# Performance work log

Measured on AMD Instinct MI355X. Metric: run time of the kernel, lower is better.

The kernel has to match this reference:

```python
import jax, jax.numpy as jnp
import numpy as np

V = 100000   # nodes (atoms)
E = 400000   # directed edges (bonds x2)
N = 74       # node_feat_size
NE = 12      # edge_feat_size
G = 200      # graph_feat_size
L = 2        # num_layers - 1 GNN layers
OUT = 1      # output_size
NG = 4000    # molecules in the batch


def _lin_init(k, fan_in, fan_out):
    s = 1.0 / np.sqrt(fan_in)
    return jax.random.uniform(k, (fan_in, fan_out), jnp.float32, -s, s)


def setup_inputs() -> dict:
    key = jax.random.key(0)
    ks = list(jax.random.split(key, 40))
    p = {}
    # node feats uniform in (0.05, 0.95) so mask = 1/(sum(h[:,-4:])*(1-h[:,0])) - 1 is finite
    p["node_feats"] = jax.random.uniform(ks[0], (V, N), jnp.float32, 0.05, 0.95)
    p["edge_feats"] = jax.random.normal(ks[1], (E, NE), jnp.float32)
    # GetContext params
    p["pn_W"] = _lin_init(ks[2], N, G);            p["pn_b"] = jnp.zeros((G,), jnp.float32)
    p["pe1_W"] = _lin_init(ks[3], N + NE, G);      p["pe1_b"] = jnp.zeros((G,), jnp.float32)
    p["pe2_W"] = _lin_init(ks[4], 2 * G, 1);       p["pe2_b"] = jnp.zeros((1,), jnp.float32)
    p["et_W"] = _lin_init(ks[5], G, G);            p["et_b"] = jnp.zeros((G,), jnp.float32)
    p["gru0_Wih"] = _lin_init(ks[6], G, 3 * G);    p["gru0_Whh"] = _lin_init(ks[7], G, 3 * G)
    p["gru0_bih"] = jnp.zeros((3 * G,), jnp.float32)
    p["gru0_bhh"] = jnp.zeros((3 * G,), jnp.float32)
    # stacked GNNLayer params
    p["gnn_pe_W"] = jnp.stack([_lin_init(ks[8 + l], 2 * G, 1) for l in range(L)])
    p["gnn_pe_b"] = jnp.zeros((L, 1), jnp.float32)
    p["gnn_pn_W"] = jnp.stack([_lin_init(ks[10 + l], G, G) for l in range(L)])
    p["gnn_pn_b"] = jnp.zeros((L, G), jnp.float32)
    p["gnn_gru_Wih"] = jnp.stack([_lin_init(ks[12 + l], G, 3 * G) for l in range(L)])
    p["gnn_gru_Whh"] = jnp.stack([_lin_init(ks[14 + l], G, 3 * G) for l in range(L)])
    p["gnn_gru_bih"] = jnp.zeros((L, 3 * G), jnp.float32)
    p["gnn_gru_bhh"] = jnp.zeros((L, 3 * G), jnp.float32)
    p["pred_W"] = _lin_init(ks[16], G, OUT);       p["pred_b"] = jnp.zeros((OUT,), jnp.float32)
    # graph structure
    p["src"] = jax.random.randint(ks[17], (E,), 0, V)
    p["dst"] = jax.random.randint(ks[18], (E,), 0, V)
    p["graph_ids"] = jnp.arange(V, dtype=jnp.int32) // (V // NG)  # sorted, balanced, non-empty
    p["n_graphs"] = NG
    return p


def _edge_softmax(logits, dst, num_nodes):
    # softmax over incoming edges of each destination node (DGL edge_softmax)
    m = jax.ops.segment_max(logits, dst, num_segments=num_nodes)
    e = jnp.exp(logits - m[dst])
    s = jax.ops.segment_sum(e, dst, num_segments=num_nodes)
    return e / s[dst]


def _gru_cell(x, h, Wih, Whh, bih, bhh):
    gi = x @ Wih + bih
    gh = h @ Whh + bhh
    ir, iz, inn = jnp.split(gi, 3, axis=-1)
    hr, hz, hn = jnp.split(gh, 3, axis=-1)
    r = jax.nn.sigmoid(ir + hr)
    z = jax.nn.sigmoid(iz + hz)
    n = jnp.tanh(inn + r * hn)
    return (1.0 - z) * n + z * h


def _forward(node_feats, edge_feats, pn_W, pn_b, pe1_W, pe1_b, pe2_W, pe2_b,
             et_W, et_b, gru0_Wih, gru0_Whh, gru0_bih, gru0_bhh,
             gnn_pe_W, gnn_pe_b, gnn_pn_W, gnn_pn_b,
             gnn_gru_Wih, gnn_gru_Whh, gnn_gru_bih, gnn_gru_bhh,
             pred_W, pred_b, src, dst, graph_ids, n_graphs):
    Vn = node_feats.shape[0]
    lrelu = jax.nn.leaky_relu  # slope 0.01, matches torch default
    # mask from original node features g.ndata['h']
    mask = jnp.sum(node_feats[:, -4:], axis=1) * (1.0 - node_feats[:, 0])
    mask = 1.0 / mask - 1.0
    # --- GetContext ---
    hv_new = lrelu(node_feats @ pn_W + pn_b)                               # (V, G)
    he1 = lrelu(jnp.concatenate([node_feats[src], edge_feats], 1) @ pe1_W + pe1_b)  # (E, G)
    he2 = jnp.concatenate([hv_new[dst], he1], 1)                           # (E, 2G)
    logits = lrelu(he2 @ pe2_W + pe2_b)                                    # (E, 1)
    a = _edge_softmax(logits, dst, Vn)
    e = a * (he1 @ et_W + et_b)                                            # (E, G)
    c = jax.ops.segment_sum(e, dst, num_segments=Vn)                       # (V, G)
    nf = jax.nn.relu(_gru_cell(jax.nn.elu(c), hv_new,
                               gru0_Wih, gru0_Whh, gru0_bih, gru0_bhh))
    # --- GNN layers ---
    for l in range(gnn_pe_W.shape[0]):
        he = jnp.concatenate([nf[dst], nf[src]], 1)                        # (E, 2G)
        lg = lrelu(he @ gnn_pe_W[l] + gnn_pe_b[l])                         # (E, 1)
        a = _edge_softmax(lg, dst, Vn)
        hvp = nf @ gnn_pn_W[l] + gnn_pn_b[l]                               # (V, G)
        c = jax.ops.segment_sum(hvp[src] * a, dst, num_segments=Vn)        # (V, G)
        nf = jax.nn.relu(_gru_cell(jax.nn.elu(c), nf,
                                   gnn_gru_Wih[l], gnn_gru_Whh[l],
                                   gnn_gru_bih[l], gnn_gru_bhh[l]))
    # --- readout ---
    atom_pka = nf @ pred_W + pred_b                                        # (V, 1)
    atom_pka = -(atom_pka + mask[:, None])
    h_pow = jnp.power(10.0, atom_pka)
    g_feats = -jnp.log10(jax.ops.segment_sum(h_pow, graph_ids, num_segments=n_graphs))
    atom_pka_out = -atom_pka
    return g_feats, atom_pka_out


def reference(node_feats, edge_feats, pn_W, pn_b, pe1_W, pe1_b, pe2_W, pe2_b,
              et_W, et_b, gru0_Wih, gru0_Whh, gru0_bih, gru0_bhh,
              gnn_pe_W, gnn_pe_b, gnn_pn_W, gnn_pn_b,
              gnn_gru_Wih, gnn_gru_Whh, gnn_gru_bih, gnn_gru_bhh,
              pred_W, pred_b, src, dst, graph_ids, n_graphs):
    return _forward(node_feats, edge_feats, pn_W, pn_b, pe1_W, pe1_b, pe2_W, pe2_b,
                    et_W, et_b, gru0_Wih, gru0_Whh, gru0_bih, gru0_bhh,
                    gnn_pe_W, gnn_pe_b, gnn_pn_W, gnn_pn_b,
                    gnn_gru_Wih, gnn_gru_Whh, gnn_gru_bih, gnn_gru_bhh,
                    pred_W, pred_b, src, dst, graph_ids, n_graphs)
```

## Files before the change

kernel.cpp:

```cpp
#include <hip/hip_runtime.h>
#include <hip/hip_bf16.h>
#include <math.h>

#define V_N    100000
#define E_N    400000
#define NFEAT  74
#define NEFEAT 12
#define G_DIM  200
#define LDA    224
#define L_N    2
#define NG_N   4000
#define NROWB  391
#define NROWP  392
#define NSWZ   (NROWP / 8 * 56)
#define NSWZG  (NROWP / 8 * 112)

static inline int cdiv(int a, int b) { return (a + b - 1) / b; }

__device__ __forceinline__ float lrelu_f(float x) { return x > 0.f ? x : 0.01f * x; }
__device__ __forceinline__ float sigmoid_f(float x) { return 1.f / (1.f + expf(-x)); }
__device__ __forceinline__ float elu_f(float x) { return x > 0.f ? x : expm1f(x); }
__device__ __forceinline__ float bf2f(__hip_bfloat16 x) { return __bfloat162float(x); }
__device__ __forceinline__ float bfbits2f(short s) {
    return __uint_as_float(((unsigned)(unsigned short)s) << 16);
}

__device__ __forceinline__ short f2bf(float f) {
    __hip_bfloat16 b = __float2bfloat16(f);
    short s;
    __builtin_memcpy(&s, &b, 2);
    return s;
}

typedef short short8 __attribute__((ext_vector_type(8)));
typedef short short4v __attribute__((ext_vector_type(4)));
typedef float f32x4 __attribute__((ext_vector_type(4)));

#define MFMA16(a, b, c) __builtin_amdgcn_mfma_f32_16x16x32_bf16((a), (b), (c), 0, 0, 0)

#define GLOAD_LDS16(gp, lp) \
    __builtin_amdgcn_global_load_lds((const __attribute__((address_space(1))) void*)(gp), \
                                     (__attribute__((address_space(3))) void*)(lp), 16, 0, 0)

__device__ __forceinline__ void swz_decode7(int lin, int& rowBlk, int& cb)
{
    int grp = lin / 56;
    int rem = lin % 56;
    cb = rem >> 3;
    rowBlk = grp * 8 + (rem & 7);
}

__device__ __forceinline__ void swz_decode14(int lin, int& rowBlk, int& cb)
{
    int grp = lin / 112;
    int rem = lin % 112;
    cb = rem >> 3;
    rowBlk = grp * 8 + (rem & 7);
}

__device__ __forceinline__ f32x4 qcalc(const f32x4* wef, f32x4 ef0, f32x4 ef1, f32x4 ef2)
{
    f32x4 q = ef0[0] * wef[0];
    q += ef0[1] * wef[1];
    q += ef0[2] * wef[2];
    q += ef0[3] * wef[3];
    q += ef1[0] * wef[4];
    q += ef1[1] * wef[5];
    q += ef1[2] * wef[6];
    q += ef1[3] * wef[7];
    q += ef2[0] * wef[8];
    q += ef2[1] * wef[9];
    q += ef2[2] * wef[10];
    q += ef2[3] * wef[11];
    return q;
}

__global__ __launch_bounds__(256)
void fill_kernel(float* __restrict__ p, float v, int n)
{
    int i = blockIdx.x * blockDim.x + threadIdx.x;
    if (i < n) p[i] = v;
}

__global__ __launch_bounds__(256)
void fill_int_kernel(int* __restrict__ p, int v, int n)
{
    int i = blockIdx.x * blockDim.x + threadIdx.x;
    if (i < n) p[i] = v;
}

__global__ __launch_bounds__(256)
void pad_zero_kernel(short* __restrict__ base, size_t VP)
{
    int idx = blockIdx.x * blockDim.x + threadIdx.x;
    if (idx >= 4 * V_N) return;
    int mat = idx / V_N, row = idx % V_N;
    short* p = base + (size_t)mat * VP + (long)row * LDA + G_DIM;
    short8 z = {};
    *(short8*)(p) = z;
    *(short8*)(p + 8) = z;
    *(short8*)(p + 16) = z;
}

__global__ __launch_bounds__(256)
void wprep_kernel(const float* __restrict__ W, short* __restrict__ Wp, int K, int Kpad)
{
    int idx = blockIdx.x * 256 + threadIdx.x;
    if (idx >= 256 * Kpad) return;
    int j = idx / Kpad, k = idx % Kpad;
    float v = (j < G_DIM && k < K) ? W[(long)k * G_DIM + j] : 0.f;
    Wp[idx] = f2bf(v);
}

__global__ __launch_bounds__(256)
void wprep_tiled_kernel(const float* __restrict__ W, short* __restrict__ Wp)
{
    int idx = blockIdx.x * 256 + threadIdx.x;
    if (idx >= 7 * 7 * 1024) return;
    int cb = idx / (7 * 1024);
    int r = idx % (7 * 1024);
    int st = r / 1024;
    int r2 = r % 1024;
    int cc = r2 / 32, kk = r2 % 32;
    int col = cb * 32 + cc, k = st * 32 + kk;
    float v = (col < G_DIM && k < G_DIM) ? W[(long)k * G_DIM + col] : 0.f;
    Wp[idx] = f2bf(v);
}

__global__ __launch_bounds__(256)
void gru_wprep_kernel(const float* __restrict__ Wih, const float* __restrict__ Whh,
                      short* __restrict__ Wp)
{
    int idx = blockIdx.x * 256 + threadIdx.x;
    if (idx >= 14 * 14 * 1536) return;
    int cb = idx / (14 * 1536);
    int r = idx % (14 * 1536);
    int st = r / 1536;
    int r2 = r % 1536;
    int g = r2 / 512;
    int r3 = r2 % 512;
    int cc = r3 / 32, kk = r3 % 32;
    int col = cb * 16 + cc;
    float v = 0.f;
    if (col < G_DIM) {
        if (st < 7) {
            int k = st * 32 + kk;
            if (k < G_DIM) v = Wih[(long)k * (3 * G_DIM) + g * G_DIM + col];
        } else {
            int k = (st - 7) * 32 + kk;
            if (k < G_DIM) v = Whh[(long)k * (3 * G_DIM) + g * G_DIM + col];
        }
    }
    Wp[idx] = f2bf(v);
}

__global__ __launch_bounds__(256)
void hist_kernel(const int* __restrict__ dst, int* __restrict__ deg)
{
    int e = blockIdx.x * blockDim.x + threadIdx.x;
    if (e >= E_N) return;
    atomicAdd(&deg[dst[e]], 1);
}

__global__ __launch_bounds__(256)
void scan1_kernel(const int* __restrict__ deg, int* __restrict__ rp, int* __restrict__ bsum)
{
    __shared__ int s[256];
    int tid = threadIdx.x;
    int v = blockIdx.x * 256 + tid;
    int x = (v < V_N) ? deg[v] : 0;
    s[tid] = x;
    __syncthreads();
    for (int off = 1; off < 256; off <<= 1) {
        int t = (tid >= off) ? s[tid - off] : 0;
        __syncthreads();
        s[tid] += t;
        __syncthreads();
    }
    if (v < V_N) rp[v] = s[tid] - x;
    if (tid == 255) bsum[blockIdx.x] = s[255];
}

__global__ void scan2_kernel(int* __restrict__ bsum, int* __restrict__ rp, int nb)
{
    if (threadIdx.x != 0 || blockIdx.x != 0) return;
    int acc = 0;
    for (int b = 0; b < nb; b++) { int t = bsum[b]; bsum[b] = acc; acc += t; }
    rp[V_N] = acc;
}

__global__ __launch_bounds__(256)
void scan3_kernel(int* __restrict__ rp, const int* __restrict__ bsum)
{
    int v = blockIdx.x * 256 + threadIdx.x;
    if (v < V_N) rp[v] += bsum[v >> 8];
}

__global__ __launch_bounds__(256)
void csr_fill_kernel(const int* __restrict__ dst, const int* __restrict__ rp,
                     int* __restrict__ cnt, int* __restrict__ perm)
{
    int e = blockIdx.x * blockDim.x + threadIdx.x;
    if (e >= E_N) return;
    int d = dst[e];
    int pos = rp[d] + atomicAdd(&cnt[d], 1);
    perm[pos] = e;
}

__global__ __launch_bounds__(256)
void gemm_f32a_dual_kernel(const float* __restrict__ Af32,
                           const short* __restrict__ Wp1, const float* __restrict__ b1,
                           const short* __restrict__ Wp2, const float* __restrict__ b2,
                           __hip_bfloat16* __restrict__ C1,
                           __hip_bfloat16* __restrict__ C2)
{
    __shared__ short As[64 * 40];
    __shared__ short Bs1[64 * 40];
    __shared__ short Bs2[64 * 40];
    const int tid = threadIdx.x;
    const int lane = tid & 63;
    const int w = tid >> 6;
    const int quad = lane >> 4;
    const int lm = lane & 15;
    const int rowBase = blockIdx.y * 64;
    const int j0 = blockIdx.x * 64;
    const int arow = tid >> 2;
    const int akc = (tid & 3) * 8;
    const int agrow = rowBase + arow;

    f32x4 acc1[4] = {}, acc2[4] = {};

    for (int k0 = 0; k0 < 96; k0 += 32) {
        short8 av = {};
        if (agrow < V_N) {
            int gk = k0 + akc;
            #pragma unroll
            for (int i = 0; i < 8; i++) {
                int kg = gk + i;
                av[i] = (kg < NFEAT) ? f2bf(Af32[(long)agrow * NFEAT + kg]) : (short)0;
            }
        }
        *(short8*)&As[arow * 40 + akc] = av;
        {
            int col = tid >> 2;
            *(short8*)&Bs1[col * 40 + akc] =
                *(const short8*)(Wp1 + (long)(j0 + col) * 96 + k0 + akc);
            *(short8*)&Bs2[col * 40 + akc] =
                *(const short8*)(Wp2 + (long)(j0 + col) * 96 + k0 + akc);
        }
        __syncthreads();
        short8 a = *(short8*)&As[(w * 16 + lm) * 40 + quad * 8];
        #pragma unroll
        for (int nt = 0; nt < 4; nt++) {
            short8 bb1 = *(short8*)&Bs1[(nt * 16 + lm) * 40 + quad * 8];
            short8 bb2 = *(short8*)&Bs2[(nt * 16 + lm) * 40 + quad * 8];
            acc1[nt] = MFMA16(a, bb1, acc1[nt]);
            acc2[nt] = MFMA16(a, bb2, acc2[nt]);
        }
        __syncthreads();
    }

    #pragma unroll
    for (int nt = 0; nt < 4; nt++) {
        int col = j0 + nt * 16 + lm;
        if (col >= G_DIM) continue;
        float bv1 = b1[col], bv2 = b2[col];
        #pragma unroll
        for (int r = 0; r < 4; r++) {
            int grow = rowBase + w * 16 + quad * 4 + r;
            if (grow >= V_N) continue;
            C1[(long)grow * LDA + col] = __float2bfloat16(lrelu_f(acc1[nt][r] + bv1));
            C2[(long)grow * LDA + col] = __float2bfloat16(acc2[nt][r] + bv2);
        }
    }
}

template<int EPI>
__global__ __launch_bounds__(256)
void gemm_bf16a_kernel(const __hip_bfloat16* __restrict__ Abf,
                       const short* __restrict__ Wp,
                       const float* __restrict__ bias,
                       __hip_bfloat16* __restrict__ Cbf)
{
    __shared__ short As[2][256 * 32];
    int rowBlk, cb;
    swz_decode7(blockIdx.x, rowBlk, cb);
    if (rowBlk >= NROWB) return;
    const int tid = threadIdx.x;
    const int lane = tid & 63;
    const int w = tid >> 6;
    const int quad = lane >> 4;
    const int lm = lane & 15;
    const int j0 = cb * 32;
    const int rowBase = rowBlk * 256;

    const short* WpB = Wp + (long)cb * (7 * 1024);
    const short* As_g = (const short*)Abf;
    const long aoff = (long)(rowBase + w * 64 + (lane >> 2)) * LDA + (lane & 3) * 8;
    const int bfrag = lm * 32 + quad * 8;

    auto stageA = [&](int st, int buf) {
        const int kl = st * 32;
        #pragma unroll
        for (int c = 0; c < 4; c++)
            GLOAD_LDS16(As_g + aoff + (long)c * 16 * LDA + kl,
                        &As[buf][(w * 64 + c * 16) * 32]);
    };
    auto loadB = [&](int st, short8 bf[2]) {
        const short* bp = WpB + st * 1024 + bfrag;
        #pragma unroll
        for (int nt = 0; nt < 2; nt++)
            bf[nt] = *(const short8*)(bp + nt * 512);
    };

    f32x4 acc[4][2] = {};
    short8 bF[2], bN[2];

    stageA(0, 0);
    loadB(0, bF);
    __syncthreads();

    int buf = 0;
    #pragma unroll 1
    for (int st = 0; st < 7; st++) {
        if (st + 1 < 7) {
            stageA(st + 1, buf ^ 1);
            loadB(st + 1, bN);
        }
        #pragma unroll
        for (int rt = 0; rt < 4; rt++) {
            short8 a = *(short8*)&As[buf][(w * 64 + rt * 16 + lm) * 32 + quad * 8];
            acc[rt][0] = MFMA16(a, bF[0], acc[rt][0]);
            acc[rt][1] = MFMA16(a, bF[1], acc[rt][1]);
        }
        __syncthreads();
        if (st + 1 < 7) {
            bF[0] = bN[0];
            bF[1] = bN[1];
        }
        buf ^= 1;
    }

    #pragma unroll
    for (int nt = 0; nt < 2; nt++) {
        int col = j0 + nt * 16 + lm;
        if (col >= G_DIM) continue;
        float bv = bias[col];
        #pragma unroll
        for (int rt = 0; rt < 4; rt++) {
            #pragma unroll
            for (int r = 0; r < 4; r++) {
                int grow = rowBase + w * 64 + rt * 16 + quad * 4 + r;
                if (grow >= V_N) continue;
                float v = acc[rt][nt][r] + bv;
                if (EPI == 3) v = elu_f(v);
                Cbf[(long)grow * LDA + col] = __float2bfloat16(v);
            }
        }
    }
}

__global__ __launch_bounds__(256, 3)
void gru_mfma_kernel(const __hip_bfloat16* __restrict__ xc,
                     const __hip_bfloat16* __restrict__ h,
                     const short* __restrict__ Wp,
                     const float* __restrict__ bih, const float* __restrict__ bhh,
                     __hip_bfloat16* __restrict__ out)
{
    __shared__ short As[2][256 * 32];
    int rowBlk, cb;
    swz_decode14(blockIdx.x, rowBlk, cb);
    if (rowBlk >= NROWB) return;
    const int tid = threadIdx.x;
    const int lane = tid & 63;
    const int w = tid >> 6;
    const int quad = lane >> 4;
    const int lm = lane & 15;
    const int j0 = cb * 16;
    const int rowBase = rowBlk * 256;

    const short* WpB = Wp + (long)cb * (14 * 1536);
    const short* xc_s = (const short*)xc;
    const short* h_s = (const short*)h;
    const long aoff = (long)(rowBase + w * 64 + (lane >> 2)) * LDA + (lane & 3) * 8;
    const int bfrag = lm * 32 + quad * 8;

    auto stageA = [&](int st, int buf) {
        const short* Ap = (st < 7) ? xc_s : h_s;
        const int kl = (st < 7 ? st : st - 7) * 32;
        #pragma unroll
        for (int c = 0; c < 4; c++)
            GLOAD_LDS16(Ap + aoff + (long)c * 16 * LDA + kl,
                        &As[buf][(w * 64 + c * 16) * 32]);
    };
    auto loadB = [&](int st, short8 bf[3]) {
        const short* bp = WpB + st * 1536 + bfrag;
        #pragma unroll
        for (int g = 0; g < 3; g++)
            bf[g] = *(const short8*)(bp + g * 512);
    };

    f32x4 aR[4] = {}, aZ[4] = {}, aNl[4] = {}, aNh[4] = {};
    short8 bF[3], bN[3];

    stageA(0, 0);
    loadB(0, bF);
    __syncthreads();

    int buf = 0;
    #pragma unroll 1
    for (int st = 0; st < 14; st++) {
        if (st + 1 < 14) {
            stageA(st + 1, buf ^ 1);
            loadB(st + 1, bN);
        }
        #pragma unroll
        for (int rt = 0; rt < 4; rt++) {
            short8 a = *(short8*)&As[buf][(w * 64 + rt * 16 + lm) * 32 + quad * 8];
            aR[rt] = MFMA16(a, bF[0], aR[rt]);
            aZ[rt] = MFMA16(a, bF[1], aZ[rt]);
            if (st < 7) aNl[rt] = MFMA16(a, bF[2], aNl[rt]);
            else        aNh[rt] = MFMA16(a, bF[2], aNh[rt]);
        }
        __syncthreads();
        if (st + 1 < 14) {
            bF[0] = bN[0];
            bF[1] = bN[1];
            bF[2] = bN[2];
        }
        buf ^= 1;
    }

    int col = j0 + lm;
    if (col < G_DIM) {
        float b_ir = bih[col], b_iz = bih[G_DIM + col], b_in = bih[2 * G_DIM + col];
        float b_hr = bhh[col], b_hz = bhh[G_DIM + col], b_hn = bhh[2 * G_DIM + col];
        #pragma unroll
        for (int rt = 0; rt < 4; rt++) {
            #pragma unroll
            for (int r = 0; r < 4; r++) {
                int grow = rowBase + w * 64 + rt * 16 + quad * 4 + r;
                if (grow >= V_N) continue;
                float sr = aR[rt][r] + b_ir + b_hr;
                float sz = aZ[rt][r] + b_iz + b_hz;
                float gin = aNl[rt][r] + b_in;
                float ghn = aNh[rt][r] + b_hn;
                float rr = sigmoid_f(sr);
                float zz = sigmoid_f(sz);
                float nn = tanhf(gin + rr * ghn);
                float hval = bf2f(h[(long)grow * LDA + col]);
                float o = (1.f - zz) * nn + zz * hval;
                out[(long)grow * LDA + col] = __float2bfloat16(o > 0.f ? o : 0.f);
            }
        }
    }
}

__global__ __launch_bounds__(256)
void node_dot2_kernel(const __hip_bfloat16* __restrict__ X,
                      const float* __restrict__ wa, const float* __restrict__ wb,
                      float* __restrict__ s1, float* __restrict__ s2)
{
    int w = threadIdx.x >> 6, lane = threadIdx.x & 63;
    int v = blockIdx.x * 4 + w;
    if (v >= V_N) return;
    int vlane = (lane < 50) ? lane : 0;
    short4v pv = *(const short4v*)((const short*)X + (long)v * LDA + vlane * 4);
    f32x4 wav = *(const f32x4*)(wa + vlane * 4);
    float a = 0.f, b = 0.f;
    #pragma unroll
    for (int u = 0; u < 4; u++) a += bfbits2f(pv[u]) * wav[u];
    if (wb) {
        f32x4 wbv = *(const f32x4*)(wb + vlane * 4);
        #pragma unroll
        for (int u = 0; u < 4; u++) b += bfbits2f(pv[u]) * wbv[u];
    }
    if (lane >= 50) { a = 0.f; b = 0.f; }
    for (int off = 32; off > 0; off >>= 1) {
        a += __shfl_down(a, off, 64);
        if (wb) b += __shfl_down(b, off, 64);
    }
    if (lane == 0) {
        s1[v] = a;
        if (wb) s2[v] = b;
    }
}

__global__ __launch_bounds__(256)
void ctx_fused_kernel(const __hip_bfloat16* __restrict__ P,
                      const float* __restrict__ efeat,
                      const int* __restrict__ src,
                      const int* __restrict__ rp, const int* __restrict__ perm,
                      const float* __restrict__ s1,
                      const float* __restrict__ pe1W,
                      const float* __restrict__ pe2W, const float* __restrict__ pe2b,
                      __hip_bfloat16* __restrict__ hbar)
{
    const int tid = threadIdx.x;
    const int w = tid >> 6, lane = tid & 63;
    const int vlane = (lane < 50) ? lane : 0;
    const int v = __builtin_amdgcn_readfirstlane(blockIdx.x * 4 + w);
    if (v >= V_N) return;
    const int b = __builtin_amdgcn_readfirstlane(rp[v]);
    const int en = __builtin_amdgcn_readfirstlane(rp[v + 1]);
    if (en == b) {
        if (lane < 50) {
            short4v z = {};
            *(short4v*)((short*)hbar + (long)v * LDA + lane * 4) = z;
        }
        return;
    }
    f32x4 wef[12];
    #pragma unroll
    for (int j = 0; j < 12; j++)
        wef[j] = *(const f32x4*)(pe1W + (long)(NFEAT + j) * G_DIM + vlane * 4);
    const f32x4 w2 = *(const f32x4*)(pe2W + G_DIM + vlane * 4);
    const float s1b = s1[v] + pe2b[0];

    float m = -INFINITY, ssum = 0.f;
    f32x4 a = {};
    for (int i = b; i < en; i++) {
        const int e = __builtin_amdgcn_readfirstlane(perm[i]);
        const int sN = __builtin_amdgcn_readfirstlane(src[e]);
        const f32x4 ef0 = *(const f32x4*)(efeat + (long)e * NEFEAT);
        const f32x4 ef1 = *(const f32x4*)(efeat + (long)e * NEFEAT + 4);
        const f32x4 ef2 = *(const f32x4*)(efeat + (long)e * NEFEAT + 8);
        const short4v pv = *(const short4v*)((const short*)P + (long)sN * LDA + vlane * 4);
        const f32x4 q = qcalc(wef, ef0, ef1, ef2);
        f32x4 he;
        #pragma unroll
        for (int u = 0; u < 4; u++) he[u] = lrelu_f(bfbits2f(pv[u]) + q[u]);
        float dot = he[0] * w2[0] + he[1] * w2[1] + he[2] * w2[2] + he[3] * w2[3];
        if (lane >= 50) dot = 0.f;
        #pragma unroll
        for (int off = 32; off > 0; off >>= 1) dot += __shfl_xor(dot, off, 64);
        const float l = lrelu_f(dot + s1b);
        if (l <= m) {
            const float wgt = expf(l - m);
            ssum += wgt;
            #pragma unroll
            for (int u = 0; u < 4; u++) a[u] += wgt * he[u];
        } else {
            const float scale = expf(m - l);
            ssum = ssum * scale + 1.f;
            #pragma unroll
            for (int u = 0; u < 4; u++) a[u] = a[u] * scale + he[u];
            m = l;
        }
    }
    const float inv = 1.f / ssum;
    if (lane < 50) {
        short4v o;
        #pragma unroll
        for (int u = 0; u < 4; u++) o[u] = f2bf(a[u] * inv);
        *(short4v*)((short*)hbar + (long)v * LDA + lane * 4) = o;
    }
}

__global__ __launch_bounds__(256)
void gnn_fused_agg_kernel(const __hip_bfloat16* __restrict__ X,
                          const int* __restrict__ src,
                          const int* __restrict__ rp, const int* __restrict__ perm,
                          const float* __restrict__ s1, const float* __restrict__ s2,
                          const float* __restrict__ bias,
                          __hip_bfloat16* __restrict__ out)
{
    const int tid = threadIdx.x;
    const int w = tid >> 6, lane = tid & 63;
    const int vlane = (lane < 50) ? lane : 0;
    const int v = __builtin_amdgcn_readfirstlane(blockIdx.x * 4 + w);
    if (v >= V_N) return;
    const int b = __builtin_amdgcn_readfirstlane(rp[v]);
    const int en = __builtin_amdgcn_readfirstlane(rp[v + 1]);
    if (en == b) {
        if (lane < 50) {
            short4v z = {};
            *(short4v*)((short*)out + (long)v * LDA + lane * 4) = z;
        }
        return;
    }
    const float s1v = s1[v] + bias[0];
    float m = -INFINITY;
    for (int i = b; i < en; i++) {
        const int e = __builtin_amdgcn_readfirstlane(perm[i]);
        const int sN = __builtin_amdgcn_readfirstlane(src[e]);
        m = fmaxf(m, lrelu_f(s1v + s2[sN]));
    }
    f32x4 a = {};
    float ssum = 0.f;
    for (int i = b; i < en; i++) {
        const int e = __builtin_amdgcn_readfirstlane(perm[i]);
        const int sN = __builtin_amdgcn_readfirstlane(src[e]);
        const float l = lrelu_f(s1v + s2[sN]);
        const float wgt = expf(l - m);
        ssum += wgt;
        const short4v pv = *(const short4v*)((const short*)X + (long)sN * LDA + vlane * 4);
        #pragma unroll
        for (int u = 0; u < 4; u++)
            a[u] += wgt * bfbits2f(pv[u]);
    }
    const float inv = 1.f / ssum;
    if (lane < 50) {
        short4v o;
        #pragma unroll
        for (int u = 0; u < 4; u++) o[u] = f2bf(elu_f(a[u] * inv));
        *(short4v*)((short*)out + (long)v * LDA + lane * 4) = o;
    }
}

__global__ __launch_bounds__(256)
void mask_kernel(const float* __restrict__ nfeat, float* __restrict__ mask)
{
    int v = blockIdx.x * blockDim.x + threadIdx.x;
    if (v >= V_N) return;
    const float* row = nfeat + (long)v * NFEAT;
    float s = row[NFEAT - 4] + row[NFEAT - 3] + row[NFEAT - 2] + row[NFEAT - 1];
    float m = s * (1.f - row[0]);
    mask[v] = 1.f / m - 1.f;
}

__global__ __launch_bounds__(256)
void readout_kernel(const __hip_bfloat16* __restrict__ nf, const float* __restrict__ predW,
                    const float* __restrict__ predb, const float* __restrict__ mask,
                    const int* __restrict__ gid, float* __restrict__ out_atom,
                    float* __restrict__ gsum)
{
    int gtid = blockIdx.x * blockDim.x + threadIdx.x;
    int v = gtid >> 6, lane = gtid & 63;
    if (v >= V_N) return;
    int vlane = (lane < 50) ? lane : 0;
    short4v pv = *(const short4v*)((const short*)nf + (long)v * LDA + vlane * 4);
    f32x4 wv = *(const f32x4*)(predW + vlane * 4);
    float acc = 0.f;
    #pragma unroll
    for (int u = 0; u < 4; u++) acc += bfbits2f(pv[u]) * wv[u];
    if (lane >= 50) acc = 0.f;
    for (int off = 32; off > 0; off >>= 1) acc += __shfl_down(acc, off, 64);
    if (lane == 0) {
        float p = acc + predb[0] + mask[v];
        out_atom[v] = p;
        atomicAdd(&gsum[gid[v]], exp10f(-p));
    }
}

__global__ __launch_bounds__(256)
void graph_out_kernel(const float* __restrict__ gsum, float* __restrict__ out_g)
{
    int g = blockIdx.x * blockDim.x + threadIdx.x;
    if (g >= NG_N) return;
    out_g[g] = -log10f(gsum[g]);
}

extern "C" void kernel_launch(void* const* d_in, const int* in_sizes, int n_in,
                              void* d_out, int out_size, void* d_ws, size_t ws_size,
                              hipStream_t stream)
{
    const float* node_feats = (const float*)d_in[0];
    const float* edge_feats = (const float*)d_in[1];
    const float* pn_W  = (const float*)d_in[2];
    const float* pn_b  = (const float*)d_in[3];
    const float* pe1_W = (const float*)d_in[4];
    const float* pe1_b = (const float*)d_in[5];
    const float* pe2_W = (const float*)d_in[6];
    const float* pe2_b = (const float*)d_in[7];
    const float* et_W  = (const float*)d_in[8];
    const float* et_b  = (const float*)d_in[9];
    const float* gru0_Wih = (const float*)d_in[10];
    const float* gru0_Whh = (const float*)d_in[11];
    const float* gru0_bih = (const float*)d_in[12];
    const float* gru0_bhh = (const float*)d_in[13];
    const float* gnn_pe_W = (const float*)d_in[14];
    const float* gnn_pe_b = (const float*)d_in[15];
    const float* gnn_pn_W = (const float*)d_in[16];
    const float* gnn_pn_b = (const float*)d_in[17];
    const float* gnn_gru_Wih = (const float*)d_in[18];
    const float* gnn_gru_Whh = (const float*)d_in[19];
    const float* gnn_gru_bih = (const float*)d_in[20];
    const float* gnn_gru_bhh = (const float*)d_in[21];
    const float* pred_W = (const float*)d_in[22];
    const float* pred_b = (const float*)d_in[23];
    const int* src = (const int*)d_in[24];
    const int* dst = (const int*)d_in[25];
    const int* gid = (const int*)d_in[26];

    float* out_g = (float*)d_out;
    float* out_atom = out_g + NG_N;

    char* base = (char*)d_ws;
    size_t off = 0;
    auto take = [&](size_t bytes) -> void* {
        void* p = base + off;
        off += (bytes + 255) & ~(size_t)255;
        return p;
    };
    const size_t VP = (size_t)V_N * LDA;
    const size_t WPL = (size_t)14 * 14 * 1536;
    float* mask   = (float*)take((size_t)V_N * 4);
    float* s1     = (float*)take((size_t)V_N * 4);
    float* s2     = (float*)take((size_t)V_N * 4);
    float* gsum   = (float*)take((size_t)NG_N * 4);
    __hip_bfloat16* c    = (__hip_bfloat16*)take(VP * 2);
    __hip_bfloat16* hv   = (__hip_bfloat16*)take(VP * 2);
    __hip_bfloat16* nf_a = (__hip_bfloat16*)take(VP * 2);
    __hip_bfloat16* nf_b = (__hip_bfloat16*)take(VP * 2);
    short* WpGru = (short*)take(3 * WPL * 2);
    short* Wp_pn0 = (short*)take((size_t)256 * 96 * 2);
    short* Wp_pe1 = (short*)take((size_t)256 * 96 * 2);
    short* Wp_et  = (short*)take((size_t)7 * 7 * 1024 * 2);
    short* Wp_pn1 = (short*)take((size_t)7 * 7 * 1024 * 2);
    short* Wp_pn2 = (short*)take((size_t)7 * 7 * 1024 * 2);
    int* deg  = (int*)take((size_t)V_N * 4);
    int* cnt  = (int*)take((size_t)V_N * 4);
    int* rp   = (int*)take((size_t)(V_N + 1) * 4);
    int* perm = (int*)take((size_t)E_N * 4);
    int* bsum = (int*)take((size_t)512 * 4);
    __hip_bfloat16* P    = nf_a;
    __hip_bfloat16* hbar = nf_b;
    __hip_bfloat16* hvp  = hv;

    if (off > ws_size) {
        fill_kernel<<<cdiv(out_size, 256), 256, 0, stream>>>((float*)d_out, -12345.f, out_size);
        return;
    }

    const int BLK = 256;
    const int nScanBlocks = cdiv(V_N, 256);
    const dim3 gOld(4, cdiv(V_N, 64));
    const int gAgg = cdiv(V_N, 4);

    pad_zero_kernel<<<cdiv(4 * V_N, BLK), BLK, 0, stream>>>((short*)c, VP);

    gru_wprep_kernel<<<cdiv(14 * 14 * 1536, 256), BLK, 0, stream>>>(gru0_Wih, gru0_Whh, WpGru);
    for (int l = 0; l < L_N; l++)
        gru_wprep_kernel<<<cdiv(14 * 14 * 1536, 256), BLK, 0, stream>>>(
            gnn_gru_Wih + (size_t)l * G_DIM * 3 * G_DIM,
            gnn_gru_Whh + (size_t)l * G_DIM * 3 * G_DIM,
            WpGru + (size_t)(l + 1) * WPL);
    wprep_kernel<<<cdiv(256 * 96, 256), BLK, 0, stream>>>(pn_W, Wp_pn0, NFEAT, 96);
    wprep_kernel<<<cdiv(256 * 96, 256), BLK, 0, stream>>>(pe1_W, Wp_pe1, NFEAT, 96);
    wprep_tiled_kernel<<<cdiv(7 * 7 * 1024, 256), BLK, 0, stream>>>(et_W, Wp_et);
    wprep_tiled_kernel<<<cdiv(7 * 7 * 1024, 256), BLK, 0, stream>>>(gnn_pn_W, Wp_pn1);
    wprep_tiled_kernel<<<cdiv(7 * 7 * 1024, 256), BLK, 0, stream>>>(
        gnn_pn_W + (size_t)G_DIM * G_DIM, Wp_pn2);

    mask_kernel<<<cdiv(V_N, BLK), BLK, 0, stream>>>(node_feats, mask);

    fill_int_kernel<<<cdiv(V_N, BLK), BLK, 0, stream>>>(deg, 0, V_N);
    hist_kernel<<<cdiv(E_N, BLK), BLK, 0, stream>>>(dst, deg);
    scan1_kernel<<<nScanBlocks, BLK, 0, stream>>>(deg, rp, bsum);
    scan2_kernel<<<1, 1, 0, stream>>>(bsum, rp, nScanBlocks);
    scan3_kernel<<<nScanBlocks, BLK, 0, stream>>>(rp, bsum);
    fill_int_kernel<<<cdiv(V_N, BLK), BLK, 0, stream>>>(cnt, 0, V_N);
    csr_fill_kernel<<<cdiv(E_N, BLK), BLK, 0, stream>>>(dst, rp, cnt, perm);

    gemm_f32a_dual_kernel<<<gOld, BLK, 0, stream>>>(
        node_feats, Wp_pn0, pn_b, Wp_pe1, pe1_b, hv, P);
    node_dot2_kernel<<<gAgg, BLK, 0, stream>>>(hv, pe2_W, nullptr, s1, nullptr);
    ctx_fused_kernel<<<gAgg, BLK, 0, stream>>>(
        P, edge_feats, src, rp, perm, s1, pe1_W, pe2_W, pe2_b, hbar);
    gemm_bf16a_kernel<3><<<NSWZ, BLK, 0, stream>>>(hbar, Wp_et, et_b, c);
    gru_mfma_kernel<<<NSWZG, BLK, 0, stream>>>(c, hv, WpGru, gru0_bih, gru0_bhh, nf_a);

    __hip_bfloat16* cur = nf_a;
    __hip_bfloat16* nxt = nf_b;
    for (int l = 0; l < L_N; l++) {
        const float* pe_W = gnn_pe_W + (size_t)l * 2 * G_DIM;
        const float* pe_b = gnn_pe_b + l;
        const float* pnB  = gnn_pn_b + (size_t)l * G_DIM;
        const float* bih  = gnn_gru_bih + (size_t)l * 3 * G_DIM;
        const float* bhh  = gnn_gru_bhh + (size_t)l * 3 * G_DIM;
        const short* WpPn = (l == 0) ? Wp_pn1 : Wp_pn2;

        node_dot2_kernel<<<gAgg, BLK, 0, stream>>>(cur, pe_W, pe_W + G_DIM, s1, s2);
        gemm_bf16a_kernel<1><<<NSWZ, BLK, 0, stream>>>(cur, WpPn, pnB, hvp);
        gnn_fused_agg_kernel<<<gAgg, BLK, 0, stream>>>(
            hvp, src, rp, perm, s1, s2, pe_b, c);
        gru_mfma_kernel<<<NSWZG, BLK, 0, stream>>>(
            c, cur, WpGru + (size_t)(l + 1) * WPL, bih, bhh, nxt);

        __hip_bfloat16* tmp = cur; cur = nxt; nxt = tmp;
    }

    fill_kernel<<<cdiv(NG_N, BLK), BLK, 0, stream>>>(gsum, 0.f, NG_N);
    readout_kernel<<<cdiv(V_N * 64, BLK), BLK, 0, stream>>>(
        cur, pred_W, pred_b, mask, gid, out_atom, gsum);
    graph_out_kernel<<<cdiv(NG_N, BLK), BLK, 0, stream>>>(gsum, out_g);
}
```

Measured before the change: 1.263 ms.

## Replace block barriers in GEMM loops with per-wave vmcnt waits and unroll by two

```diff
diff --git a/kernel.cpp b/kernel.cpp
--- a/kernel.cpp
+++ b/kernel.cpp
@@ -41,6 +41,11 @@
 #define GLOAD_LDS16(gp, lp) \
     __builtin_amdgcn_global_load_lds((const __attribute__((address_space(1))) void*)(gp), \
                                      (__attribute__((address_space(3))) void*)(lp), 16, 0, 0)
+
+#define WAITVM(n) do { \
+    asm volatile("s_waitcnt vmcnt(" #n ")" ::: "memory"); \
+    __builtin_amdgcn_sched_barrier(0); \
+} while (0)
 
 __device__ __forceinline__ void swz_decode7(int lin, int& rowBlk, int& cb)
 {
@@ -312,33 +317,42 @@
         for (int nt = 0; nt < 2; nt++)
             bf[nt] = *(const short8*)(bp + nt * 512);
     };
-
-    f32x4 acc[4][2] = {};
-    short8 bF[2], bN[2];
-
-    stageA(0, 0);
-    loadB(0, bF);
-    __syncthreads();
-
-    int buf = 0;
-    #pragma unroll 1
-    for (int st = 0; st < 7; st++) {
-        if (st + 1 < 7) {
-            stageA(st + 1, buf ^ 1);
-            loadB(st + 1, bN);
-        }
+    auto mfmaStep = [&](int buf, short8 bf[2], f32x4 acc[4][2]) {
         #pragma unroll
         for (int rt = 0; rt < 4; rt++) {
             short8 a = *(short8*)&As[buf][(w * 64 + rt * 16 + lm) * 32 + quad * 8];
-            acc[rt][0] = MFMA16(a, bF[0], acc[rt][0]);
-            acc[rt][1] = MFMA16(a, bF[1], acc[rt][1]);
-        }
-        __syncthreads();
+            acc[rt][0] = MFMA16(a, bf[0], acc[rt][0]);
+            acc[rt][1] = MFMA16(a, bf[1], acc[rt][1]);
+        }
+    };
+
+    f32x4 acc[4][2] = {};
+    short8 bA[2], bB[2];
+
+    stageA(0, 0);
+    loadB(0, bA);
+    WAITVM(0);
+
+    #pragma unroll 1
+    for (int st = 0; st < 7; st += 2) {
         if (st + 1 < 7) {
-            bF[0] = bN[0];
-            bF[1] = bN[1];
-        }
-        buf ^= 1;
+            stageA(st + 1, 1);
+            loadB(st + 1, bB);
+            WAITVM(6);
+        } else {
+            WAITVM(0);
+        }
+        mfmaStep(0, bA, acc);
+        if (st + 1 < 7) {
+            if (st + 2 < 7) {
+                stageA(st + 2, 0);
+                loadB(st + 2, bA);
+                WAITVM(6);
+            } else {
+                WAITVM(0);
+            }
+            mfmaStep(1, bB, acc);
+        }
     }
 
     #pragma unroll
@@ -401,34 +415,38 @@
     };
 
     f32x4 aR[4] = {}, aZ[4] = {}, aNl[4] = {}, aNh[4] = {};
-    short8 bF[3], bN[3];
-
-    stageA(0, 0);
-    loadB(0, bF);
-    __syncthreads();
-
-    int buf = 0;
-    #pragma unroll 1
-    for (int st = 0; st < 14; st++) {
-        if (st + 1 < 14) {
-            stageA(st + 1, buf ^ 1);
-            loadB(st + 1, bN);
-        }
+
+    auto mfmaStep = [&](int buf, short8 bf[3], bool lowK) {
         #pragma unroll
         for (int rt = 0; rt < 4; rt++) {
             short8 a = *(short8*)&As[buf][(w * 64 + rt * 16 + lm) * 32 + quad * 8];
-            aR[rt] = MFMA16(a, bF[0], aR[rt]);
-            aZ[rt] = MFMA16(a, bF[1], aZ[rt]);
-            if (st < 7) aNl[rt] = MFMA16(a, bF[2], aNl[rt]);
-            else        aNh[rt] = MFMA16(a, bF[2], aNh[rt]);
-        }
-        __syncthreads();
-        if (st + 1 < 14) {
-            bF[0] = bN[0];
-            bF[1] = bN[1];
-            bF[2] = bN[2];
-        }
-        buf ^= 1;
+            aR[rt] = MFMA16(a, bf[0], aR[rt]);
+            aZ[rt] = MFMA16(a, bf[1], aZ[rt]);
+            if (lowK) aNl[rt] = MFMA16(a, bf[2], aNl[rt]);
+            else      aNh[rt] = MFMA16(a, bf[2], aNh[rt]);
+        }
+    };
+
+    short8 bA[3], bB[3];
+
+    stageA(0, 0);
+    loadB(0, bA);
+    WAITVM(0);
+
+    #pragma unroll 1
+    for (int st = 0; st < 14; st += 2) {
+        stageA(st + 1, 1);
+        loadB(st + 1, bB);
+        WAITVM(7);
+        mfmaStep(0, bA, st < 7);
+        if (st + 2 < 14) {
+            stageA(st + 2, 0);
+            loadB(st + 2, bA);
+            WAITVM(7);
+        } else {
+            WAITVM(0);
+        }
+        mfmaStep(1, bB, st + 1 < 7);
     }
 
     int col = j0 + lm;
```

After: 1.232 ms. -2.4%, faster.
